# Performance work log

Measured on AMD Instinct MI355X. Metric: run time of the kernel, lower is better.

The kernel has to match this reference:

```python
import jax, jax.numpy as jnp
import numpy as np

N_HEAD = 12


def setup_inputs() -> dict:
    key = jax.random.key(0)
    ks = jax.random.split(key, 5)
    B, T, C = 2, 2048, 768
    x = jax.random.normal(ks[0], (B, T, C), dtype=jnp.float32)
    w_attn = jax.random.normal(ks[1], (3 * C, C), dtype=jnp.float32) * 0.02
    b_attn = jax.random.normal(ks[2], (3 * C,), dtype=jnp.float32) * 0.02
    w_proj = jax.random.normal(ks[3], (C, C), dtype=jnp.float32) * 0.02
    b_proj = jax.random.normal(ks[4], (C,), dtype=jnp.float32) * 0.02
    return {"x": x, "w_attn": w_attn, "b_attn": b_attn, "w_proj": w_proj, "b_proj": b_proj}


def reference(x, w_attn, b_attn, w_proj, b_proj):
    B, T, C = x.shape
    H = N_HEAD
    D = C // H
    # fused QKV projection (torch Linear: x @ W.T + b)
    qkv = x @ w_attn.T + b_attn                      # [B, T, 3C]
    q, k, v = jnp.split(qkv, 3, axis=-1)
    q = q.reshape(B, T, H, D).transpose(0, 2, 1, 3)  # [B, H, T, D]
    k = k.reshape(B, T, H, D).transpose(0, 2, 1, 3)
    v = v.reshape(B, T, H, D).transpose(0, 2, 1, 3)
    # NOTE: original scales by 1/sqrt(k.size(0)) == 1/sqrt(B) (batch!), reproduced faithfully
    scale = 1.0 / jnp.sqrt(jnp.asarray(B, dtype=x.dtype))
    scores = jnp.einsum("bhtd,bhsd->bhts", q, k) * scale  # [B, H, T, T]
    causal = jnp.tril(jnp.ones((T, T), dtype=bool))
    scores = jnp.where(causal[None, None], scores, jnp.asarray(-jnp.inf, dtype=x.dtype))
    attn = jax.nn.softmax(scores, axis=-1)
    # dropout layers are identity in eval mode
    out = jnp.einsum("bhts,bhsd->bhtd", attn, v)     # [B, H, T, D]
    out = out.transpose(0, 2, 1, 3).reshape(B, T, C)
    return out @ w_proj.T + b_proj
```

## Files before the change

### kernel.cpp

```cpp
#include <hip/hip_runtime.h>
#include <hip/hip_bf16.h>
#include <stdint.h>

typedef __bf16 bf16;
typedef __bf16 bf16x4 __attribute__((ext_vector_type(4)));
typedef __bf16 bf16x8 __attribute__((ext_vector_type(8)));
typedef float f32x4 __attribute__((ext_vector_type(4)));

__device__ __forceinline__ f32x4 mfma16(bf16x8 a, bf16x8 b, f32x4 c) {
    return __builtin_amdgcn_mfma_f32_16x16x32_bf16(a, b, c, 0, 0, 0);
}

__device__ __forceinline__ void gload_lds16(const void* g, void* l) {
    __builtin_amdgcn_global_load_lds((__attribute__((address_space(1))) void*)g,
                                     (__attribute__((address_space(3))) void*)l,
                                     16, 0, 0);
}

__global__ void k_cast3(const float* __restrict__ x, const float* __restrict__ wa,
                        const float* __restrict__ wp, bf16* __restrict__ xb,
                        bf16* __restrict__ wab, bf16* __restrict__ wpb) {
    const int N1 = 786432, N2 = 442368, N3 = 147456;
    int i = blockIdx.x * blockDim.x + threadIdx.x;
    int stride = gridDim.x * blockDim.x;
    for (; i < N1 + N2 + N3; i += stride) {
        const float* src; bf16* dst; int j = i;
        if (j < N1)           { src = x;  dst = xb; }
        else if (j < N1 + N2) { src = wa; dst = wab; j -= N1; }
        else                  { src = wp; dst = wpb; j -= N1 + N2; }
        float4 v = reinterpret_cast<const float4*>(src)[j];
        bf16x4 o = { (bf16)v.x, (bf16)v.y, (bf16)v.z, (bf16)v.w };
        reinterpret_cast<bf16x4*>(dst)[j] = o;
    }
}

template<int BN, bool BF16_OUT>
__global__ __launch_bounds__(256) void k_gemm_bt(
        const bf16* __restrict__ A, const bf16* __restrict__ W,
        const float* __restrict__ bias, void* __restrict__ Cout,
        int M, int N, int K) {
    constexpr int FN = BN / 32;
    __shared__ bf16 As[128 * 64];
    __shared__ bf16 Ws[BN * 64];
    const int tid = threadIdx.x;
    const int l = tid & 63, w = tid >> 6;
    const int lr = l & 15, lq = l >> 4;
    const int wm = w >> 1, wn = w & 1;

    const int nwg = gridDim.x;
    const int q8 = nwg >> 3;
    const int swz = (blockIdx.x & 7) * q8 + (blockIdx.x >> 3);
    const int nbx = N / BN;
    const int bm = (swz / nbx) * 128, bn = (swz % nbx) * BN;

    f32x4 acc[4][FN] = {};

    for (int k0 = 0; k0 < K; k0 += 64) {
        __syncthreads();
        #pragma unroll
        for (int i = 0; i < 4; ++i) {
            int c = tid + i * 256;
            int row = c >> 3, j = c & 7;
            int src8 = (j ^ (row & 7)) * 8;
            gload_lds16(A + (size_t)(bm + row) * K + k0 + src8, As + c * 8);
        }
        #pragma unroll
        for (int i = 0; i < FN; ++i) {
            int c = tid + i * 256;
            int row = c >> 3, j = c & 7;
            int src8 = (j ^ (row & 7)) * 8;
            gload_lds16(W + (size_t)(bn + row) * K + k0 + src8, Ws + c * 8);
        }
        __syncthreads();
        bf16x8 af[2][4], wf[2][FN];
        #pragma unroll
        for (int ks = 0; ks < 2; ++ks) {
            #pragma unroll
            for (int f = 0; f < 4; ++f) {
                int ra = wm * 64 + f * 16 + lr;
                af[ks][f] = *reinterpret_cast<const bf16x8*>(
                    As + ra * 64 + (((ks * 4 + lq) ^ (lr & 7)) * 8));
            }
            #pragma unroll
            for (int f = 0; f < FN; ++f) {
                int rb = wn * (FN * 16) + f * 16 + lr;
                wf[ks][f] = *reinterpret_cast<const bf16x8*>(
                    Ws + rb * 64 + (((ks * 4 + lq) ^ (lr & 7)) * 8));
            }
        }
        #pragma unroll
        for (int ks = 0; ks < 2; ++ks)
            #pragma unroll
            for (int fm = 0; fm < 4; ++fm)
                #pragma unroll
                for (int fn = 0; fn < FN; ++fn)
                    acc[fm][fn] = mfma16(af[ks][fm], wf[ks][fn], acc[fm][fn]);
    }

    #pragma unroll
    for (int fm = 0; fm < 4; ++fm) {
        #pragma unroll
        for (int fn = 0; fn < FN; ++fn) {
            int row = bm + wm * 64 + fm * 16 + lq * 4;
            int col = bn + wn * (FN * 16) + fn * 16 + lr;
            float bv = bias[col];
            #pragma unroll
            for (int r = 0; r < 4; ++r) {
                float v = acc[fm][fn][r] + bv;
                if (BF16_OUT)
                    ((bf16*)Cout)[(size_t)(row + r) * N + col] = (bf16)v;
                else
                    ((float*)Cout)[(size_t)(row + r) * N + col] = v;
            }
        }
    }
}

__global__ __launch_bounds__(256) void k_transV(const bf16* __restrict__ qkv,
                                                bf16* __restrict__ vT) {
    const int g = blockIdx.x;
    const int bh = g >> 4, tc = g & 15;
    const int h = bh % 12, b = bh / 12;
    const int t0 = tc * 128;
    __shared__ bf16 Lt[128][68];
    const bf16* src = qkv + (size_t)(b * 2048 + t0) * 2304 + 1536 + h * 64;
    const int tid = threadIdx.x;
    #pragma unroll
    for (int ii = 0; ii < 4; ++ii) {
        int tt = ii * 32 + (tid >> 3);
        int ch = tid & 7;
        bf16x8 v = *reinterpret_cast<const bf16x8*>(src + (size_t)tt * 2304 + ch * 8);
        union { bf16x8 v8; bf16x4 h4[2]; } u; u.v8 = v;
        *reinterpret_cast<bf16x4*>(&Lt[tt][ch * 8])     = u.h4[0];
        *reinterpret_cast<bf16x4*>(&Lt[tt][ch * 8 + 4]) = u.h4[1];
    }
    __syncthreads();
    bf16* dst = vT + (size_t)bh * 64 * 2048 + t0;
    const int d = tid >> 2;
    #pragma unroll
    for (int ii = 0; ii < 4; ++ii) {
        int tch = ii * 4 + (tid & 3);
        bf16x8 v;
        #pragma unroll
        for (int e = 0; e < 8; ++e) v[e] = Lt[tch * 8 + e][d];
        *reinterpret_cast<bf16x8*>(&dst[(size_t)d * 2048 + tch * 8]) = v;
    }
}

#define CLOG2E 1.02014439f

__global__ __launch_bounds__(256, 4) void k_flash_attn(
        const bf16* __restrict__ qkv, const bf16* __restrict__ vT,
        bf16* __restrict__ att, float* __restrict__ part, int mode) {
    __shared__ bf16 Ks[3][4096];
    __shared__ bf16 VTs[2][4096];

    const int tid = threadIdx.x;
    const int l = tid & 63, w = tid >> 6;
    const int lr = l & 15, lq = l >> 4;
    const int qh = w >> 1, hv = w & 1;

    const int bid = blockIdx.x;
    int qb, h, b, jt0, jt1, slot;
    bool dopart;
    if (mode) {
        int bh = bid % 24, idx = bid / 24;
        h = bh % 12; b = bh / 12;
        if (idx < 16)      { qb = 16 + idx;  jt0 = 0;  jt1 = 16;     dopart = true;  slot = (bh * 16 + idx) * 2; }
        else if (idx < 32) { qb = 47 - idx;  jt0 = 16; jt1 = qb + 1; dopart = true;  slot = (bh * 16 + (qb - 16)) * 2 + 1; }
        else               { qb = 47 - idx;  jt0 = 0;  jt1 = qb + 1; dopart = false; slot = 0; }
    } else {
        const int s = bid >> 8, i = (bid >> 3) & 31, t7 = bid & 7;
        if (s == 0)      qb = i;
        else if (s == 2) qb = (i + 16) & 31;
        else             qb = (i < 8) ? (31 - 2 * i) : (i < 16) ? (30 - 2 * i)
                           : (i < 24) ? (62 - 2 * i) : (63 - 2 * i);
        const int hb = s * 8 + t7;
        h = hb % 12; b = hb / 12;
        jt0 = 0; jt1 = qb + 1; dopart = false; slot = 0;
    }

    const bf16* Qp  = qkv + (size_t)b * 2048 * 2304 + h * 64;
    const bf16* Kp  = Qp + 768;
    const bf16* Vtp = vT + (size_t)(b * 12 + h) * 64 * 2048;

    bf16x8 qf[2][2];
    #pragma unroll
    for (int qg = 0; qg < 2; ++qg)
        #pragma unroll
        for (int ks = 0; ks < 2; ++ks)
            qf[qg][ks] = *reinterpret_cast<const bf16x8*>(
                Qp + (size_t)(qb * 64 + qh * 32 + qg * 16 + lr) * 2304 + ks * 32 + lq * 8);

    f32x4 o[2][4] = {};
    float lsum0 = 0.f, lsum1 = 0.f;

    auto stageK = [&](int buf, int kv0) {
        #pragma unroll
        for (int ii = 0; ii < 2; ++ii) {
            int c = tid + ii * 256;
            int row = c >> 3, j = c & 7;
            gload_lds16(Kp + (size_t)(kv0 + row) * 2304 + ((j ^ (row & 7)) * 8),
                        &Ks[buf][c * 8]);
        }
    };
    auto stageV = [&](int buf, int kv0) {
        #pragma unroll
        for (int ii = 0; ii < 2; ++ii) {
            int c = tid + ii * 256;
            int row = c >> 3, j = c & 7;
            gload_lds16(Vtp + (size_t)row * 2048 + kv0 + ((j ^ (row & 7)) * 8),
                        &VTs[buf][c * 8]);
        }
    };

    stageK(0, jt0 * 64);
    stageV(0, jt0 * 64);
    const bool two = (jt1 > jt0 + 1);
    if (two) stageK(1, jt0 * 64 + 64);
    if (two) asm volatile("s_waitcnt vmcnt(2)" ::: "memory");
    else     asm volatile("s_waitcnt vmcnt(0)" ::: "memory");
    __builtin_amdgcn_s_barrier();
    asm volatile("" ::: "memory");

    const int rsw = lr & 7;

    for (int jt = jt0; jt < jt1; ++jt) {
        const int curK = (jt - jt0) % 3;
        const int curV = (jt - jt0) & 1;
        const int kv0 = jt * 64;
        if (jt + 1 < jt1) stageV(curV ^ 1, kv0 + 64);
        if (jt + 2 < jt1) stageK((jt + 2 - jt0) % 3, kv0 + 128);

        const bool diag = (jt == qb);
        float p[2][2][4];
        __builtin_amdgcn_s_setprio(1);
        #pragma unroll
        for (int tp = 0; tp < 2; ++tp) {
            const int row = hv * 32 + tp * 16 + lr;
            bf16x8 kf0 = *reinterpret_cast<const bf16x8*>(
                &Ks[curK][row * 64 + ((lq ^ rsw) * 8)]);
            bf16x8 kf1 = *reinterpret_cast<const bf16x8*>(
                &Ks[curK][row * 64 + (((4 + lq) ^ rsw) * 8)]);
            #pragma unroll
            for (int qg = 0; qg < 2; ++qg) {
                f32x4 s = {0.f, 0.f, 0.f, 0.f};
                s = mfma16(kf0, qf[qg][0], s);
                s = mfma16(kf1, qf[qg][1], s);
                #pragma unroll
                for (int r = 0; r < 4; ++r)
                    p[tp][qg][r] = __builtin_amdgcn_exp2f(s[r] * CLOG2E);
            }
        }
        __builtin_amdgcn_s_setprio(0);
        if (diag) {
            #pragma unroll
            for (int tp = 0; tp < 2; ++tp)
                #pragma unroll
                for (int qg = 0; qg < 2; ++qg)
                    #pragma unroll
                    for (int r = 0; r < 4; ++r)
                        if (hv * 32 + tp * 16 + lq * 4 + r > qh * 32 + qg * 16 + lr)
                            p[tp][qg][r] = 0.f;
        }
        {
            float a0 = (p[0][0][0] + p[0][0][1]) + (p[0][0][2] + p[0][0][3]);
            float a1 = (p[1][0][0] + p[1][0][1]) + (p[1][0][2] + p[1][0][3]);
            lsum0 += a0 + a1;
            float b0 = (p[0][1][0] + p[0][1][1]) + (p[0][1][2] + p[0][1][3]);
            float b1 = (p[1][1][0] + p[1][1][1]) + (p[1][1][2] + p[1][1][3]);
            lsum1 += b0 + b1;
        }

        bf16x8 pa[2];
        #pragma unroll
        for (int qg = 0; qg < 2; ++qg) {
            unsigned A0, B0, A1, B1;
            asm("v_cvt_pk_bf16_f32 %0, %1, %2" : "=v"(A0) : "v"(p[0][qg][0]), "v"(p[0][qg][1]));
            asm("v_cvt_pk_bf16_f32 %0, %1, %2" : "=v"(A1) : "v"(p[0][qg][2]), "v"(p[0][qg][3]));
            asm("v_cvt_pk_bf16_f32 %0, %1, %2" : "=v"(B0) : "v"(p[1][qg][0]), "v"(p[1][qg][1]));
            asm("v_cvt_pk_bf16_f32 %0, %1, %2" : "=v"(B1) : "v"(p[1][qg][2]), "v"(p[1][qg][3]));
            asm volatile("v_permlane32_swap_b32 %0, %1" : "+v"(A0), "+v"(B0));
            asm volatile("v_permlane16_swap_b32 %0, %1" : "+v"(A0), "+v"(B0));
            asm volatile("v_permlane32_swap_b32 %0, %1" : "+v"(A1), "+v"(B1));
            asm volatile("v_permlane16_swap_b32 %0, %1" : "+v"(A1), "+v"(B1));
            union { unsigned u[4]; bf16x8 v8; } pk_;
            pk_.u[0] = A0; pk_.u[1] = A1; pk_.u[2] = B0; pk_.u[3] = B1;
            pa[qg] = pk_.v8;
        }

        __builtin_amdgcn_s_setprio(1);
        #pragma unroll
        for (int db = 0; db < 4; ++db) {
            const int row = db * 16 + lr;
            bf16x8 vf = *reinterpret_cast<const bf16x8*>(
                &VTs[curV][row * 64 + (((hv * 4 + lq) ^ rsw) * 8)]);
            o[0][db] = mfma16(pa[0], vf, o[0][db]);
            o[1][db] = mfma16(pa[1], vf, o[1][db]);
        }
        __builtin_amdgcn_s_setprio(0);

        if (jt + 1 < jt1) {
            if (jt + 2 < jt1) asm volatile("s_waitcnt vmcnt(2)" ::: "memory");
            else              asm volatile("s_waitcnt vmcnt(0)" ::: "memory");
        }
        __builtin_amdgcn_s_barrier();
        asm volatile("" ::: "memory");
    }

    lsum0 += __shfl_xor(lsum0, 16); lsum0 += __shfl_xor(lsum0, 32);
    lsum1 += __shfl_xor(lsum1, 16); lsum1 += __shfl_xor(lsum1, 32);

    {
        float* xf = (float*)&Ks[0][0];
        float* rg = xf + (size_t)(qh * 64 + l) * 34;
        if (hv == 1) {
            #pragma unroll
            for (int qg = 0; qg < 2; ++qg)
                #pragma unroll
                for (int db = 0; db < 4; ++db)
                    #pragma unroll
                    for (int r = 0; r < 4; ++r)
                        rg[qg * 16 + db * 4 + r] = o[qg][db][r];
            rg[32] = lsum0; rg[33] = lsum1;
        }
        __syncthreads();
        if (hv == 0) {
            #pragma unroll
            for (int qg = 0; qg < 2; ++qg)
                #pragma unroll
                for (int db = 0; db < 4; ++db)
                    #pragma unroll
                    for (int r = 0; r < 4; ++r)
                        o[qg][db][r] += rg[qg * 16 + db * 4 + r];
            lsum0 += rg[32]; lsum1 += rg[33];

            if (dopart) {
                float* pb = part + (size_t)slot * 4160;
                #pragma unroll
                for (int qg = 0; qg < 2; ++qg) {
                    #pragma unroll
                    for (int db = 0; db < 4; ++db)
                        #pragma unroll
                        for (int r = 0; r < 4; ++r)
                            pb[(qh * 32 + qg * 16 + lq * 4 + r) * 64 + db * 16 + lr] = o[qg][db][r];
                }
                if (lq == 0) {
                    pb[4096 + qh * 32 + lr]      = lsum0;
                    pb[4096 + qh * 32 + 16 + lr] = lsum1;
                }
            } else {
                float inv0[4], inv1[4];
                #pragma unroll
                for (int r = 0; r < 4; ++r) {
                    inv0[r] = 1.0f / __shfl(lsum0, lq * 4 + r);
                    inv1[r] = 1.0f / __shfl(lsum1, lq * 4 + r);
                }
                #pragma unroll
                for (int db = 0; db < 4; ++db)
                    #pragma unroll
                    for (int r = 0; r < 4; ++r) {
                        int q0 = qb * 64 + qh * 32 + lq * 4 + r;
                        att[(size_t)(b * 2048 + q0) * 768 + h * 64 + db * 16 + lr] =
                            (bf16)(o[0][db][r] * inv0[r]);
                        att[(size_t)(b * 2048 + q0 + 16) * 768 + h * 64 + db * 16 + lr] =
                            (bf16)(o[1][db][r] * inv1[r]);
                    }
            }
        }
    }
}

__global__ __launch_bounds__(256) void k_attn_reduce(
        const float* __restrict__ part, bf16* __restrict__ att) {
    int g = blockIdx.x;
    int bh = g / 16, q16 = g % 16, qb = 16 + q16;
    int h = bh % 12, b = bh / 12;
    const float* p0 = part + (size_t)((bh * 16 + q16) * 2) * 4160;
    const float* p1 = p0 + 4160;
    for (int e = threadIdx.x; e < 4096; e += 256) {
        int row = e >> 6, col = e & 63;
        float O = p0[e] + p1[e];
        float L = p0[4096 + row] + p1[4096 + row];
        att[(size_t)(b * 2048 + qb * 64 + row) * 768 + h * 64 + col] = (bf16)(O / L);
    }
}

extern "C" void kernel_launch(void* const* d_in, const int* in_sizes, int n_in,
                              void* d_out, int out_size, void* d_ws, size_t ws_size,
                              hipStream_t stream) {
    const float* x      = (const float*)d_in[0];
    const float* w_attn = (const float*)d_in[1];
    const float* b_attn = (const float*)d_in[2];
    const float* w_proj = (const float*)d_in[3];
    const float* b_proj = (const float*)d_in[4];

    char* ws = (char*)d_ws;
    bf16* xb   = (bf16*)(ws + 0);
    bf16* vT   = (bf16*)(ws + 0);
    bf16* wab  = (bf16*)(ws + 6291456);
    bf16* wpb  = (bf16*)(ws + 9830400);
    bf16* qkv  = (bf16*)(ws + 11010048);
    bf16* att  = (bf16*)(ws + 29884416);
    float* part = (float*)(ws + 36175872);
    const unsigned long long WS_NEEDED = 36175872ull + 12779520ull;

    k_cast3<<<2048, 256, 0, stream>>>(x, w_attn, w_proj, xb, wab, wpb);

    k_gemm_bt<128, true><<<576, 256, 0, stream>>>(xb, wab, b_attn, qkv, 4096, 2304, 768);

    k_transV<<<384, 256, 0, stream>>>(qkv, vT);

    if (ws_size >= WS_NEEDED) {
        k_flash_attn<<<1152, 256, 0, stream>>>(qkv, vT, att, part, 1);
        k_attn_reduce<<<384, 256, 0, stream>>>(part, att);
    } else {
        k_flash_attn<<<768, 256, 0, stream>>>(qkv, vT, att, part, 0);
    }

    k_gemm_bt<64, false><<<384, 256, 0, stream>>>(att, wpb, b_proj, d_out, 4096, 768, 768);
}
```

Baseline: 84.97 us.

## Double-buffer LDS tiles in GEMM to overlap global loads with MFMA

The bf16 GEMM kernel now uses two LDS buffers for the A and W tiles. The next K-tile is prefetched with global_load_lds while MFMAs run on the current tile, and a wait plus barrier at the end of each iteration replaces the two syncthreads per iteration. It also raises wave priority around the MFMA block with s_setprio. The cost is twice the LDS footprint, which may lower occupancy. The ds_reads of the current buffer rely on the end-of-iteration barrier for ordering against the async loads.

```diff
diff --git a/kernel.cpp b/kernel.cpp
--- a/kernel.cpp
+++ b/kernel.cpp
@@ -40,8 +40,8 @@
         const float* __restrict__ bias, void* __restrict__ Cout,
         int M, int N, int K) {
     constexpr int FN = BN / 32;
-    __shared__ bf16 As[128 * 64];
-    __shared__ bf16 Ws[BN * 64];
+    __shared__ bf16 As[2][128 * 64];
+    __shared__ bf16 Ws[2][BN * 64];
     const int tid = threadIdx.x;
     const int l = tid & 63, w = tid >> 6;
     const int lr = l & 15, lq = l >> 4;
@@ -53,25 +53,35 @@
     const int nbx = N / BN;
     const int bm = (swz / nbx) * 128, bn = (swz % nbx) * BN;
 
-    f32x4 acc[4][FN] = {};
-
-    for (int k0 = 0; k0 < K; k0 += 64) {
-        __syncthreads();
+    auto stage = [&](int buf, int k0) {
         #pragma unroll
         for (int i = 0; i < 4; ++i) {
             int c = tid + i * 256;
             int row = c >> 3, j = c & 7;
             int src8 = (j ^ (row & 7)) * 8;
-            gload_lds16(A + (size_t)(bm + row) * K + k0 + src8, As + c * 8);
+            gload_lds16(A + (size_t)(bm + row) * K + k0 + src8, &As[buf][c * 8]);
         }
         #pragma unroll
         for (int i = 0; i < FN; ++i) {
             int c = tid + i * 256;
             int row = c >> 3, j = c & 7;
             int src8 = (j ^ (row & 7)) * 8;
-            gload_lds16(W + (size_t)(bn + row) * K + k0 + src8, Ws + c * 8);
-        }
-        __syncthreads();
+            gload_lds16(W + (size_t)(bn + row) * K + k0 + src8, &Ws[buf][c * 8]);
+        }
+    };
+
+    f32x4 acc[4][FN] = {};
+    const int NK = K >> 6;
+
+    stage(0, 0);
+    asm volatile("s_waitcnt vmcnt(0)" ::: "memory");
+    __builtin_amdgcn_s_barrier();
+    asm volatile("" ::: "memory");
+
+    for (int kk = 0; kk < NK; ++kk) {
+        const int cur = kk & 1;
+        if (kk + 1 < NK) stage(cur ^ 1, (kk + 1) * 64);
+
         bf16x8 af[2][4], wf[2][FN];
         #pragma unroll
         for (int ks = 0; ks < 2; ++ks) {
@@ -79,15 +89,16 @@
             for (int f = 0; f < 4; ++f) {
                 int ra = wm * 64 + f * 16 + lr;
                 af[ks][f] = *reinterpret_cast<const bf16x8*>(
-                    As + ra * 64 + (((ks * 4 + lq) ^ (lr & 7)) * 8));
+                    &As[cur][ra * 64 + (((ks * 4 + lq) ^ (lr & 7)) * 8)]);
             }
             #pragma unroll
             for (int f = 0; f < FN; ++f) {
                 int rb = wn * (FN * 16) + f * 16 + lr;
                 wf[ks][f] = *reinterpret_cast<const bf16x8*>(
-                    Ws + rb * 64 + (((ks * 4 + lq) ^ (lr & 7)) * 8));
+                    &Ws[cur][rb * 64 + (((ks * 4 + lq) ^ (lr & 7)) * 8)]);
             }
         }
+        __builtin_amdgcn_s_setprio(1);
         #pragma unroll
         for (int ks = 0; ks < 2; ++ks)
             #pragma unroll
@@ -95,6 +106,11 @@
                 #pragma unroll
                 for (int fn = 0; fn < FN; ++fn)
                     acc[fm][fn] = mfma16(af[ks][fm], wf[ks][fn], acc[fm][fn]);
+        __builtin_amdgcn_s_setprio(0);
+
+        if (kk + 1 < NK) asm volatile("s_waitcnt vmcnt(0)" ::: "memory");
+        __builtin_amdgcn_s_barrier();
+        asm volatile("" ::: "memory");
     }
 
     #pragma unroll
```

New measurement: 92.57 us. 1.09x slower.

## Fuse split-KV partial reduction into flash attention via atomic counter

Applied to the files above, without the earlier changes.

Removes the separate reduce kernel launch. A per-tile atomic counter in workspace lets whichever of the two split blocks finishes last combine both partial outputs and normalisers and write the final attention rows. This costs an extra memset launch, thread fences and an atomic, and the last-finishing block now does the reduction serially at its tail.

```diff
diff --git a/kernel.cpp b/kernel.cpp
--- a/kernel.cpp
+++ b/kernel.cpp
@@ -151,7 +151,8 @@
 
 __global__ __launch_bounds__(256, 4) void k_flash_attn(
         const bf16* __restrict__ qkv, const bf16* __restrict__ vT,
-        bf16* __restrict__ att, float* __restrict__ part, int mode) {
+        bf16* __restrict__ att, float* __restrict__ part,
+        unsigned* __restrict__ cnt, int mode) {
     __shared__ bf16 Ks[3][4096];
     __shared__ bf16 VTs[2][4096];
 
@@ -369,20 +370,28 @@
             }
         }
     }
-}
-
-__global__ __launch_bounds__(256) void k_attn_reduce(
-        const float* __restrict__ part, bf16* __restrict__ att) {
-    int g = blockIdx.x;
-    int bh = g / 16, q16 = g % 16, qb = 16 + q16;
-    int h = bh % 12, b = bh / 12;
-    const float* p0 = part + (size_t)((bh * 16 + q16) * 2) * 4160;
-    const float* p1 = p0 + 4160;
-    for (int e = threadIdx.x; e < 4096; e += 256) {
-        int row = e >> 6, col = e & 63;
-        float O = p0[e] + p1[e];
-        float L = p0[4096 + row] + p1[4096 + row];
-        att[(size_t)(b * 2048 + qb * 64 + row) * 768 + h * 64 + col] = (bf16)(O / L);
+
+    if (dopart) {
+        const int cidx = (b * 12 + h) * 16 + (qb - 16);
+        __threadfence();
+        __syncthreads();
+        volatile int* flag = (volatile int*)&VTs[0][0];
+        if (tid == 0) {
+            unsigned old = atomicAdd(&cnt[cidx], 1u);
+            *flag = (old == 1);
+        }
+        __syncthreads();
+        if (*flag) {
+            __threadfence();
+            const float* p0 = part + (size_t)(cidx * 2) * 4160;
+            const float* p1 = p0 + 4160;
+            for (int e = tid; e < 4096; e += 256) {
+                int row = e >> 6, col = e & 63;
+                float O = p0[e] + p1[e];
+                float L = p0[4096 + row] + p1[4096 + row];
+                att[(size_t)(b * 2048 + qb * 64 + row) * 768 + h * 64 + col] = (bf16)(O / L);
+            }
+        }
     }
 }
 
@@ -403,7 +412,8 @@
     bf16* qkv  = (bf16*)(ws + 11010048);
     bf16* att  = (bf16*)(ws + 29884416);
     float* part = (float*)(ws + 36175872);
-    const unsigned long long WS_NEEDED = 36175872ull + 12779520ull;
+    unsigned* cnt = (unsigned*)(ws + 48955392);
+    const unsigned long long WS_NEEDED = 48955392ull + 1536ull;
 
     k_cast3<<<2048, 256, 0, stream>>>(x, w_attn, w_proj, xb, wab, wpb);
 
@@ -412,10 +422,10 @@
     k_transV<<<384, 256, 0, stream>>>(qkv, vT);
 
     if (ws_size >= WS_NEEDED) {
-        k_flash_attn<<<1152, 256, 0, stream>>>(qkv, vT, att, part, 1);
-        k_attn_reduce<<<384, 256, 0, stream>>>(part, att);
+        hipMemsetAsync(cnt, 0, 1536, stream);
+        k_flash_attn<<<1152, 256, 0, stream>>>(qkv, vT, att, part, cnt, 1);
     } else {
-        k_flash_attn<<<768, 256, 0, stream>>>(qkv, vT, att, part, 0);
+        k_flash_attn<<<768, 256, 0, stream>>>(qkv, vT, att, part, cnt, 0);
     }
 
     k_gemm_bt<64, false><<<384, 256, 0, stream>>>(att, wpb, b_proj, d_out, 4096, 768, 768);
```

Measured after the change: 220.5 us. 2.6x slower.
